# Kernel tuning notes

Hardware: AMD Instinct MI355X
Metric: run time of the kernel (lower is better)

## Reference

```python
import jax, jax.numpy as jnp
import numpy as np

H = 16
MAX_SEQ_LEN = 2048
B = 1
S = 2048


def setup_inputs() -> dict:
    key = jax.random.key(0)
    k1, k2, k3 = jax.random.split(key, 3)
    # int8-valued attention scores (stored as int32; values centered in [-64, 63])
    x_q = jax.random.randint(k1, (B, H, S, S), 0, 127, dtype=jnp.int32) - 64
    # per-(head, row) dequant scale for the scores
    scale_x = 0.005 + 0.015 * jax.random.uniform(k2, (H, MAX_SEQ_LEN), dtype=jnp.float32)
    # per-(head, row) requant scale for the softmax output (probs in [0,1], so ~1/127)
    scale_out = 0.004 + 0.006 * jax.random.uniform(k3, (H, MAX_SEQ_LEN), dtype=jnp.float32)
    return {"x_q": x_q, "scale_x": scale_x, "scale_out": scale_out}


def reference(x_q, scale_x, scale_out):
    seq_len = x_q.shape[-1]
    sx = scale_x[:, :seq_len]   # [H, S] per-row dequant scale
    so = scale_out[:, :seq_len]  # [H, S] per-row requant scale
    # dequantize: x[b,h,i,j] = x_q[b,h,i,j] * sx[h,i]
    x = x_q.astype(jnp.float32) * sx[None, :, :, None]
    # causal (tril) mask over the last dim
    mask = jnp.tril(jnp.ones((seq_len, seq_len), dtype=bool))  # [S, S]
    logits = jnp.where(mask[None, None, :, :], x, -jnp.inf)
    p = jax.nn.softmax(logits, axis=-1)
    # symmetric int8 requantization with per-(head, row) scale
    out_q = jnp.clip(jnp.round(p / so[None, :, :, None]), -128, 127).astype(jnp.int8)
    return (out_q, so)
```

## Files before the change

### kernel.cpp

```cpp
#include <hip/hip_runtime.h>
#include <math.h>

constexpr int S = 2048;
constexpr int HS = 16 * S;
constexpr long long OUTQ_ELEMS = (long long)HS * S;

typedef int   vint4   __attribute__((ext_vector_type(4)));
typedef float vfloat4 __attribute__((ext_vector_type(4)));

__global__ __launch_bounds__(256) void softmax_quant_wave_kernel(
    const int*   __restrict__ x_q,
    const float* __restrict__ scale_x,
    const float* __restrict__ scale_out,
    float*       __restrict__ out_q,
    float*       __restrict__ so_out)
{
    const int tid  = threadIdx.x;
    const int lane = tid & 63;
    const int wave = tid >> 6;
    const int row  = blockIdx.x * 4 + wave;
    const int i    = row & (S - 1);

    const float sx = scale_x[row];
    const float so = scale_out[row];
    const float c  = sx * 1.4426950408889634f;

    const int*  rowp = x_q   + (size_t)row * S;
    float*      outp = out_q + (size_t)row * S;

    vint4 q[8];
    #pragma unroll
    for (int ch = 0; ch < 8; ++ch) {
        const int j0 = ch * 256 + lane * 4;
        q[ch] = (vint4)(0);
        if (j0 <= i)
            q[ch] = __builtin_nontemporal_load(
                      reinterpret_cast<const vint4*>(rowp + j0));
    }

    float e[8][4];
    float s = 0.0f;
    #pragma unroll
    for (int ch = 0; ch < 8; ++ch) {
        const int j0 = ch * 256 + lane * 4;
        e[ch][0] = (j0 + 0 <= i) ? __builtin_amdgcn_exp2f((float)q[ch].x * c) : 0.0f;
        e[ch][1] = (j0 + 1 <= i) ? __builtin_amdgcn_exp2f((float)q[ch].y * c) : 0.0f;
        e[ch][2] = (j0 + 2 <= i) ? __builtin_amdgcn_exp2f((float)q[ch].z * c) : 0.0f;
        e[ch][3] = (j0 + 3 <= i) ? __builtin_amdgcn_exp2f((float)q[ch].w * c) : 0.0f;
        s += (e[ch][0] + e[ch][1]) + (e[ch][2] + e[ch][3]);
    }

    #pragma unroll
    for (int off = 32; off > 0; off >>= 1)
        s += __shfl_xor(s, off, 64);

    const float scale = 1.0f / (s * so);

    #pragma unroll
    for (int ch = 0; ch < 8; ++ch) {
        const int j0 = ch * 256 + lane * 4;
        vfloat4 o;
        o.x = fminf(rintf(e[ch][0] * scale), 127.0f);
        o.y = fminf(rintf(e[ch][1] * scale), 127.0f);
        o.z = fminf(rintf(e[ch][2] * scale), 127.0f);
        o.w = fminf(rintf(e[ch][3] * scale), 127.0f);
        __builtin_nontemporal_store(o, reinterpret_cast<vfloat4*>(outp + j0));
    }

    if (lane == 0) so_out[row] = so;
}

extern "C" void kernel_launch(void* const* d_in, const int* in_sizes, int n_in,
                              void* d_out, int out_size, void* d_ws, size_t ws_size,
                              hipStream_t stream) {
    const int*   x_q       = (const int*)d_in[0];
    const float* scale_x   = (const float*)d_in[1];
    const float* scale_out = (const float*)d_in[2];

    float* out    = (float*)d_out;
    float* so_out = out + OUTQ_ELEMS;

    dim3 grid(HS / 4);
    dim3 block(256);
    softmax_quant_wave_kernel<<<grid, block, 0, stream>>>(
        x_q, scale_x, scale_out, out, so_out);
}
```

Before: 76.25 us.

## Process two rows per block with block-wide reduction instead of one row per wave

```diff
diff --git a/kernel.cpp b/kernel.cpp
--- a/kernel.cpp
+++ b/kernel.cpp
@@ -8,7 +8,7 @@
 typedef int   vint4   __attribute__((ext_vector_type(4)));
 typedef float vfloat4 __attribute__((ext_vector_type(4)));
 
-__global__ __launch_bounds__(256) void softmax_quant_wave_kernel(
+__global__ __launch_bounds__(256) void softmax_quant_2row_kernel(
     const int*   __restrict__ x_q,
     const float* __restrict__ scale_x,
     const float* __restrict__ scale_out,
@@ -16,58 +16,98 @@
     float*       __restrict__ so_out)
 {
     const int tid  = threadIdx.x;
-    const int lane = tid & 63;
-    const int wave = tid >> 6;
-    const int row  = blockIdx.x * 4 + wave;
-    const int i    = row & (S - 1);
+    const int rowA = blockIdx.x * 2;
+    const int rowB = rowA + 1;
+    const int iA   = rowA & (S - 1);
+    const int iB   = iA + 1;
 
-    const float sx = scale_x[row];
-    const float so = scale_out[row];
-    const float c  = sx * 1.4426950408889634f;
+    const float sxA = scale_x[rowA];
+    const float sxB = scale_x[rowB];
+    const float soA = scale_out[rowA];
+    const float soB = scale_out[rowB];
+    const float cA  = sxA * 1.4426950408889634f;
+    const float cB  = sxB * 1.4426950408889634f;
 
-    const int*  rowp = x_q   + (size_t)row * S;
-    float*      outp = out_q + (size_t)row * S;
+    const int* rowpA = x_q + (size_t)rowA * S;
+    const int* rowpB = x_q + (size_t)rowB * S;
 
-    vint4 q[8];
+    const int j0 = tid * 4;
+    const int j1 = j0 + (S / 2);
+
+    vint4 qa0 = (vint4)(0), qa1 = (vint4)(0);
+    vint4 qb0 = (vint4)(0), qb1 = (vint4)(0);
+    if (j0 <= iA) qa0 = __builtin_nontemporal_load(
+                          reinterpret_cast<const vint4*>(rowpA + j0));
+    if (j1 <= iA) qa1 = __builtin_nontemporal_load(
+                          reinterpret_cast<const vint4*>(rowpA + j1));
+    if (j0 <= iB) qb0 = __builtin_nontemporal_load(
+                          reinterpret_cast<const vint4*>(rowpB + j0));
+    if (j1 <= iB) qb1 = __builtin_nontemporal_load(
+                          reinterpret_cast<const vint4*>(rowpB + j1));
+
+    float ea[8], eb[8];
+    ea[0] = (j0 + 0 <= iA) ? __builtin_amdgcn_exp2f((float)qa0.x * cA) : 0.0f;
+    ea[1] = (j0 + 1 <= iA) ? __builtin_amdgcn_exp2f((float)qa0.y * cA) : 0.0f;
+    ea[2] = (j0 + 2 <= iA) ? __builtin_amdgcn_exp2f((float)qa0.z * cA) : 0.0f;
+    ea[3] = (j0 + 3 <= iA) ? __builtin_amdgcn_exp2f((float)qa0.w * cA) : 0.0f;
+    ea[4] = (j1 + 0 <= iA) ? __builtin_amdgcn_exp2f((float)qa1.x * cA) : 0.0f;
+    ea[5] = (j1 + 1 <= iA) ? __builtin_amdgcn_exp2f((float)qa1.y * cA) : 0.0f;
+    ea[6] = (j1 + 2 <= iA) ? __builtin_amdgcn_exp2f((float)qa1.z * cA) : 0.0f;
+    ea[7] = (j1 + 3 <= iA) ? __builtin_amdgcn_exp2f((float)qa1.w * cA) : 0.0f;
+    eb[0] = (j0 + 0 <= iB) ? __builtin_amdgcn_exp2f((float)qb0.x * cB) : 0.0f;
+    eb[1] = (j0 + 1 <= iB) ? __builtin_amdgcn_exp2f((float)qb0.y * cB) : 0.0f;
+    eb[2] = (j0 + 2 <= iB) ? __builtin_amdgcn_exp2f((float)qb0.z * cB) : 0.0f;
+    eb[3] = (j0 + 3 <= iB) ? __builtin_amdgcn_exp2f((float)qb0.w * cB) : 0.0f;
+    eb[4] = (j1 + 0 <= iB) ? __builtin_amdgcn_exp2f((float)qb1.x * cB) : 0.0f;
+    eb[5] = (j1 + 1 <= iB) ? __builtin_amdgcn_exp2f((float)qb1.y * cB) : 0.0f;
+    eb[6] = (j1 + 2 <= iB) ? __builtin_amdgcn_exp2f((float)qb1.z * cB) : 0.0f;
+    eb[7] = (j1 + 3 <= iB) ? __builtin_amdgcn_exp2f((float)qb1.w * cB) : 0.0f;
+
+    float sa = ((ea[0] + ea[1]) + (ea[2] + ea[3])) + ((ea[4] + ea[5]) + (ea[6] + ea[7]));
+    float sb = ((eb[0] + eb[1]) + (eb[2] + eb[3])) + ((eb[4] + eb[5]) + (eb[6] + eb[7]));
+
     #pragma unroll
-    for (int ch = 0; ch < 8; ++ch) {
-        const int j0 = ch * 256 + lane * 4;
-        q[ch] = (vint4)(0);
-        if (j0 <= i)
-            q[ch] = __builtin_nontemporal_load(
-                      reinterpret_cast<const vint4*>(rowp + j0));
+    for (int off = 32; off > 0; off >>= 1) {
+        sa += __shfl_xor(sa, off, 64);
+        sb += __shfl_xor(sb, off, 64);
     }
 
-    float e[8][4];
-    float s = 0.0f;
-    #pragma unroll
-    for (int ch = 0; ch < 8; ++ch) {
-        const int j0 = ch * 256 + lane * 4;
-        e[ch][0] = (j0 + 0 <= i) ? __builtin_amdgcn_exp2f((float)q[ch].x * c) : 0.0f;
-        e[ch][1] = (j0 + 1 <= i) ? __builtin_amdgcn_exp2f((float)q[ch].y * c) : 0.0f;
-        e[ch][2] = (j0 + 2 <= i) ? __builtin_amdgcn_exp2f((float)q[ch].z * c) : 0.0f;
-        e[ch][3] = (j0 + 3 <= i) ? __builtin_amdgcn_exp2f((float)q[ch].w * c) : 0.0f;
-        s += (e[ch][0] + e[ch][1]) + (e[ch][2] + e[ch][3]);
-    }
+    __shared__ float red[4][2];
+    const int wave = tid >> 6;
+    if ((tid & 63) == 0) { red[wave][0] = sa; red[wave][1] = sb; }
+    __syncthreads();
+    sa = (red[0][0] + red[1][0]) + (red[2][0] + red[3][0]);
+    sb = (red[0][1] + red[1][1]) + (red[2][1] + red[3][1]);
 
-    #pragma unroll
-    for (int off = 32; off > 0; off >>= 1)
-        s += __shfl_xor(s, off, 64);
+    const float scaleA = 1.0f / (sa * soA);
+    const float scaleB = 1.0f / (sb * soB);
 
-    const float scale = 1.0f / (s * so);
+    float* outpA = out_q + (size_t)rowA * S;
+    float* outpB = out_q + (size_t)rowB * S;
 
-    #pragma unroll
-    for (int ch = 0; ch < 8; ++ch) {
-        const int j0 = ch * 256 + lane * 4;
-        vfloat4 o;
-        o.x = fminf(rintf(e[ch][0] * scale), 127.0f);
-        o.y = fminf(rintf(e[ch][1] * scale), 127.0f);
-        o.z = fminf(rintf(e[ch][2] * scale), 127.0f);
-        o.w = fminf(rintf(e[ch][3] * scale), 127.0f);
-        __builtin_nontemporal_store(o, reinterpret_cast<vfloat4*>(outp + j0));
-    }
+    vfloat4 o;
+    o.x = fminf(rintf(ea[0] * scaleA), 127.0f);
+    o.y = fminf(rintf(ea[1] * scaleA), 127.0f);
+    o.z = fminf(rintf(ea[2] * scaleA), 127.0f);
+    o.w = fminf(rintf(ea[3] * scaleA), 127.0f);
+    __builtin_nontemporal_store(o, reinterpret_cast<vfloat4*>(outpA + j0));
+    o.x = fminf(rintf(ea[4] * scaleA), 127.0f);
+    o.y = fminf(rintf(ea[5] * scaleA), 127.0f);
+    o.z = fminf(rintf(ea[6] * scaleA), 127.0f);
+    o.w = fminf(rintf(ea[7] * scaleA), 127.0f);
+    __builtin_nontemporal_store(o, reinterpret_cast<vfloat4*>(outpA + j1));
+    o.x = fminf(rintf(eb[0] * scaleB), 127.0f);
+    o.y = fminf(rintf(eb[1] * scaleB), 127.0f);
+    o.z = fminf(rintf(eb[2] * scaleB), 127.0f);
+    o.w = fminf(rintf(eb[3] * scaleB), 127.0f);
+    __builtin_nontemporal_store(o, reinterpret_cast<vfloat4*>(outpB + j0));
+    o.x = fminf(rintf(eb[4] * scaleB), 127.0f);
+    o.y = fminf(rintf(eb[5] * scaleB), 127.0f);
+    o.z = fminf(rintf(eb[6] * scaleB), 127.0f);
+    o.w = fminf(rintf(eb[7] * scaleB), 127.0f);
+    __builtin_nontemporal_store(o, reinterpret_cast<vfloat4*>(outpB + j1));
 
-    if (lane == 0) so_out[row] = so;
+    if (tid == 0) { so_out[rowA] = soA; so_out[rowB] = soB; }
 }
 
 extern "C" void kernel_launch(void* const* d_in, const int* in_sizes, int n_in,
@@ -80,8 +120,8 @@
     float* out    = (float*)d_out;
     float* so_out = out + OUTQ_ELEMS;
 
-    dim3 grid(HS / 4);
+    dim3 grid(HS / 2);
     dim3 block(256);
-    softmax_quant_wave_kernel<<<grid, block, 0, stream>>>(
+    softmax_quant_2row_kernel<<<grid, block, 0, stream>>>(
         x_q, scale_x, scale_out, out, so_out);
 }
```

New measurement: 73.44 us. 1.04x faster.
